# Kernel optimization log

Measured on AMD Instinct MI355X. Metric: run time of the kernel, lower is better.

Reference implementation:

```python
import jax, jax.numpy as jnp
import numpy as np

T, B, E, H, R = 1024, 8, 1024, 16, 16
HD = E // H


def setup_inputs() -> dict:
    key = jax.random.key(0)
    ks = jax.random.split(key, 10)
    w = lambda k, shape: (jax.random.normal(k, shape, jnp.float32) * 0.02)
    return {
        "query": jax.random.normal(ks[0], (T, B, E), jnp.float32),
        "in_proj_weight": w(ks[1], (3 * E, E)),
        "in_proj_bias": jnp.zeros((3 * E,), jnp.float32),
        "in_left": w(ks[2], (3 * E, R)),   # LrkLinear(rank -> 3E) weight
        "in_right": w(ks[3], (R, E)),      # LrkLinear(E -> rank) weight
        "out_proj_weight": w(ks[4], (E, E)),
        "out_proj_bias": jnp.zeros((E,), jnp.float32),
        "out_left": w(ks[5], (E, R)),
        "out_right": w(ks[6], (R, E)),
        "rel_pos_bias": w(ks[7], (H, T, T)),
    }


def reference(query, in_proj_weight, in_proj_bias, in_left, in_right,
              out_proj_weight, out_proj_bias, out_left, out_right, rel_pos_bias):
    t, b, e = query.shape
    hd = e // H
    scaling = float(hd) ** -0.5
    # fused in-projection: residual full-rank + low-rank branch
    acti = (jnp.einsum('tbe,fe->tbf', query, in_proj_weight) + in_proj_bias
            + jnp.einsum('tbr,fr->tbf', jnp.einsum('tbe,re->tbr', query, in_right), in_left))
    q, k, v = jnp.split(acti, 3, axis=-1)
    q = q * scaling
    # (T,B,E) -> (B,H,T,hd); matches torch view(T, B*H, hd).transpose(0,1)
    to_heads = lambda x: x.reshape(t, b, H, hd).transpose(1, 2, 0, 3)
    qh, kh, vh = to_heads(q), to_heads(k), to_heads(v)
    scores = jnp.einsum('bhtd,bhsd->bhts', qh, kh) + rel_pos_bias  # bias broadcasts over batch
    attn = jax.nn.softmax(scores, axis=-1)  # dropout_p = 0
    out = jnp.einsum('bhts,bhsd->bhtd', attn, vh)
    out = out.transpose(2, 0, 1, 3).reshape(t, b, e)
    # out-projection: residual full-rank + low-rank branch
    out = (jnp.einsum('tbe,fe->tbf', out, out_proj_weight) + out_proj_bias
           + jnp.einsum('tbr,fr->tbf', jnp.einsum('tbe,re->tbr', out, out_right), out_left))
    return out
```

## Files before the change

kernel.cpp:

```cpp
#include <hip/hip_runtime.h>
#include <hip/hip_bf16.h>


typedef __attribute__((ext_vector_type(8))) __bf16 bf16x8;
typedef __attribute__((ext_vector_type(4))) float f32x4;

__device__ __forceinline__ float bf2f(unsigned short u) {
  union { unsigned int i; float f; } v; v.i = ((unsigned int)u) << 16; return v.f;
}
__device__ __forceinline__ unsigned short f2bf(float f) {
  union { float f; unsigned int i; } v; v.f = f;
  unsigned int x = v.i;
  unsigned int r = x + 0x7FFFu + ((x >> 16) & 1u);
  return (unsigned short)(r >> 16);
}
__device__ __forceinline__ unsigned int pack2(float a, float b) {
  return (unsigned int)f2bf(a) | ((unsigned int)f2bf(b) << 16);
}
__device__ __forceinline__ float ld_in(const void* p, long idx, int isf32) {
  if (isf32) return ((const float*)p)[idx];
  return bf2f(((const unsigned short*)p)[idx]);
}
__device__ __forceinline__ void gl_lds16(const unsigned short* g, unsigned short* l) {
  __builtin_amdgcn_global_load_lds(
      (const __attribute__((address_space(1))) unsigned int*)g,
      (__attribute__((address_space(3))) unsigned int*)l, 16, 0, 0);
}

__global__ void detect_kernel(const unsigned int* __restrict__ q, int* __restrict__ flag) {
  __shared__ int cnt;
  if (threadIdx.x == 0) cnt = 0;
  __syncthreads();
  unsigned int w = q[threadIdx.x];
  int c = 0;
  if (((w >> 7) & 0xFFu) >= 0xC0u) c++;
  if (((w >> 23) & 0xFFu) >= 0xC0u) c++;
  atomicAdd(&cnt, c);
  __syncthreads();
  if (threadIdx.x == 0) flag[0] = (cnt >= 2) ? 1 : 0;
}

__global__ __launch_bounds__(256) void convert_bf16(
    const void* __restrict__ in, unsigned short* __restrict__ out,
    const int* __restrict__ flag) {
  long idx = ((long)blockIdx.x * 256 + threadIdx.x) * 8;
  if (flag[0]) {
    const float* p = (const float*)in + idx;
    float4 a = ((const float4*)p)[0], b = ((const float4*)p)[1];
    uint4 v;
    v.x = pack2(a.x, a.y); v.y = pack2(a.z, a.w);
    v.z = pack2(b.x, b.y); v.w = pack2(b.z, b.w);
    *(uint4*)(out + idx) = v;
  } else {
    *(uint4*)(out + idx) = *(const uint4*)((const unsigned short*)in + idx);
  }
}

__global__ __launch_bounds__(256) void eff_weights(
    const void* __restrict__ w, const void* __restrict__ left,
    const void* __restrict__ right, unsigned short* __restrict__ outw,
    const int* __restrict__ flag) {
  const int isf32 = flag[0];
  long idx = (long)blockIdx.x * 256 + threadIdx.x;
  long f = idx >> 10, e = idx & 1023;
  float acc = ld_in(w, idx, isf32);
#pragma unroll
  for (int r = 0; r < 16; ++r)
    acc += ld_in(left, (f << 4) + r, isf32) * ld_in(right, (r << 10) + e, isf32);
  outw[idx] = f2bf(acc);
}

__global__ __launch_bounds__(256) void inproj_kernel(
    const unsigned short* __restrict__ qbf,
    const unsigned short* __restrict__ weff,
    const void* __restrict__ bias,
    unsigned short* __restrict__ qh, unsigned short* __restrict__ kh,
    unsigned short* __restrict__ vt, const int* __restrict__ flag) {
  __shared__ __align__(16) unsigned short As[128 * 32];
  __shared__ __align__(16) unsigned short Bs[128 * 32];
  const int isf32 = flag[0];
  const int tid = threadIdx.x;
  const int wave = tid >> 6, lane = tid & 63, quad = lane >> 4, lrow = lane & 15;
  const int wr0 = (wave >> 1) * 64, wc0 = (wave & 1) * 64;
  const int fbase = blockIdx.x * 128, mbase = blockIdx.y * 128;
  const int srow = lane >> 2, scol = (lane & 3) * 8;
  const unsigned short* ag  = qbf  + (long)(mbase + 32 * wave + srow) * 1024 + scol;
  const unsigned short* ag2 = ag + 16 * 1024;
  const unsigned short* bg  = weff + (long)(fbase + 32 * wave + srow) * 1024 + scol;
  const unsigned short* bg2 = bg + 16 * 1024;
  unsigned short* la  = &As[(32 * wave) * 32];
  unsigned short* la2 = &As[(32 * wave + 16) * 32];
  unsigned short* lb  = &Bs[(32 * wave) * 32];
  unsigned short* lb2 = &Bs[(32 * wave + 16) * 32];

  f32x4 acc[4][4] = {};
  for (int k0 = 0; k0 < 1024; k0 += 32) {
    gl_lds16(ag + k0, la);
    gl_lds16(ag2 + k0, la2);
    gl_lds16(bg + k0, lb);
    gl_lds16(bg2 + k0, lb2);
    __syncthreads();
    bf16x8 af[4], bfv[4];
#pragma unroll
    for (int mi = 0; mi < 4; ++mi)
      af[mi] = *(const bf16x8*)&As[(wr0 + mi * 16 + lrow) * 32 + quad * 8];
#pragma unroll
    for (int ni = 0; ni < 4; ++ni)
      bfv[ni] = *(const bf16x8*)&Bs[(wc0 + ni * 16 + lrow) * 32 + quad * 8];
#pragma unroll
    for (int mi = 0; mi < 4; ++mi)
#pragma unroll
      for (int ni = 0; ni < 4; ++ni)
        acc[mi][ni] = __builtin_amdgcn_mfma_f32_16x16x32_bf16(af[mi], bfv[ni], acc[mi][ni], 0, 0, 0);
    __syncthreads();
  }
  const int which = fbase >> 10;
  const int h = ((fbase + wc0) >> 6) & 15;
#pragma unroll
  for (int ni = 0; ni < 4; ++ni) {
    const int d = ni * 16 + lrow;
    const float bv = ld_in(bias, fbase + wc0 + d, isf32);
#pragma unroll
    for (int mi = 0; mi < 4; ++mi)
#pragma unroll
      for (int r = 0; r < 4; ++r) {
        const int m = mbase + wr0 + mi * 16 + quad * 4 + r;
        const int t = m >> 3, b = m & 7;
        const float val = acc[mi][ni][r] + bv;
        if (which == 0)
          qh[((long)(b * 16 + h) * 1024 + t) * 64 + d] = f2bf(val * 0.125f);
        else if (which == 1)
          kh[((long)(b * 16 + h) * 1024 + t) * 64 + d] = f2bf(val);
        else
          vt[((long)(b * 16 + h) * 64 + d) * 1024 + t] = f2bf(val);
      }
  }
}

__global__ __launch_bounds__(256) void attn_kernel(
    const unsigned short* __restrict__ qh, const unsigned short* __restrict__ kh,
    const unsigned short* __restrict__ vt, const void* __restrict__ rpb,
    const unsigned short* __restrict__ pre,
    unsigned short* __restrict__ ctx, const int* __restrict__ flag) {
  __shared__ __align__(16) unsigned short Ks[2 * 64 * 32];
  __shared__ __align__(16) unsigned short Ps[4][16][72];
  const int isf32 = flag[0];
  const int tid = threadIdx.x;
  const int wave = tid >> 6, lane = tid & 63, quad = lane >> 4, lrow = lane & 15;
  const int bh = blockIdx.y, b = bh >> 4, h = bh & 15;
  const int t0 = blockIdx.x * 64;

  const unsigned short* qbase = qh + ((long)(bh * 1024) + t0 + wave * 16 + lrow) * 64;
  bf16x8 qf0 = *(const bf16x8*)(qbase + quad * 8);
  bf16x8 qf1 = *(const bf16x8*)(qbase + 32 + quad * 8);

  const unsigned short* kbase = kh + (long)bh * 65536;
  const unsigned short* vbase = vt + (long)bh * 65536;

  const long bidx0 = ((long)h * 1024 + t0 + wave * 16 + quad * 4) * 1024 + lrow;
  const unsigned short* bs16 = pre ? pre : (const unsigned short*)rpb;
  const bool bf32 = (isf32 && pre == nullptr);
  const float* bsf = (const float*)rpb;

  const int j0 = 2 * wave, j1 = 2 * wave + 1;
  const int kk0 = j0 >> 2, ii0 = j0 & 3, kk1 = j1 >> 2, ii1 = j1 & 3;
  const unsigned short* kg0 = kbase + (long)(16 * ii0 + (lane >> 2)) * 64 + kk0 * 32 + (lane & 3) * 8;
  const unsigned short* kg1 = kbase + (long)(16 * ii1 + (lane >> 2)) * 64 + kk1 * 32 + (lane & 3) * 8;
  unsigned short* lk0 = &Ks[kk0 * 2048 + ii0 * 512];
  unsigned short* lk1 = &Ks[kk1 * 2048 + ii1 * 512];

  f32x4 oacc[4] = {};
  float rsum[4] = {0.f, 0.f, 0.f, 0.f};

  for (int s0 = 0; s0 < 1024; s0 += 64) {
    gl_lds16(kg0 + (long)s0 * 64, lk0);
    gl_lds16(kg1 + (long)s0 * 64, lk1);
    __syncthreads();

    float bia[4][4];
    if (bf32) {
#pragma unroll
      for (int r = 0; r < 4; ++r)
#pragma unroll
        for (int n = 0; n < 4; ++n)
          bia[r][n] = bsf[bidx0 + r * 1024 + s0 + n * 16];
    } else {
#pragma unroll
      for (int r = 0; r < 4; ++r)
#pragma unroll
        for (int n = 0; n < 4; ++n)
          bia[r][n] = bf2f(bs16[bidx0 + r * 1024 + s0 + n * 16]);
    }

    f32x4 sacc[4] = {};
#pragma unroll
    for (int n = 0; n < 4; ++n) {
      bf16x8 kf0 = *(const bf16x8*)&Ks[(n * 16 + lrow) * 32 + quad * 8];
      bf16x8 kf1 = *(const bf16x8*)&Ks[2048 + (n * 16 + lrow) * 32 + quad * 8];
      sacc[n] = __builtin_amdgcn_mfma_f32_16x16x32_bf16(qf0, kf0, sacc[n], 0, 0, 0);
      sacc[n] = __builtin_amdgcn_mfma_f32_16x16x32_bf16(qf1, kf1, sacc[n], 0, 0, 0);
    }

#pragma unroll
    for (int n = 0; n < 4; ++n)
#pragma unroll
      for (int r = 0; r < 4; ++r) {
        float p = __expf(sacc[n][r] + bia[r][n]);
        rsum[r] += p;
        Ps[wave][quad * 4 + r][n * 16 + lrow] = f2bf(p);
      }

    asm volatile("s_waitcnt lgkmcnt(0)" ::: "memory");

#pragma unroll
    for (int kk = 0; kk < 2; ++kk) {
      bf16x8 pf = *(const bf16x8*)&Ps[wave][lrow][kk * 32 + quad * 8];
#pragma unroll
      for (int n = 0; n < 4; ++n) {
        bf16x8 vf = *(const bf16x8*)(vbase + (long)(n * 16 + lrow) * 1024 + s0 + kk * 32 + quad * 8);
        oacc[n] = __builtin_amdgcn_mfma_f32_16x16x32_bf16(pf, vf, oacc[n], 0, 0, 0);
      }
    }
    __syncthreads();
  }

#pragma unroll
  for (int msk = 1; msk <= 8; msk <<= 1)
#pragma unroll
    for (int r = 0; r < 4; ++r)
      rsum[r] += __shfl_xor(rsum[r], msk, 64);

  float linv[4];
#pragma unroll
  for (int r = 0; r < 4; ++r) linv[r] = 1.0f / rsum[r];
#pragma unroll
  for (int n = 0; n < 4; ++n)
#pragma unroll
    for (int r = 0; r < 4; ++r) {
      const int t = t0 + wave * 16 + quad * 4 + r;
      ctx[((long)t * 8 + b) * 1024 + h * 64 + n * 16 + lrow] = f2bf(oacc[n][r] * linv[r]);
    }
}

__global__ __launch_bounds__(256) void outproj_kernel(
    const unsigned short* __restrict__ ctx, const unsigned short* __restrict__ weff,
    const void* __restrict__ bias, void* __restrict__ out,
    const int* __restrict__ flag) {
  __shared__ __align__(16) unsigned short As[128 * 32];
  __shared__ __align__(16) unsigned short Bs[128 * 32];
  const int isf32 = flag[0];
  const int tid = threadIdx.x;
  const int wave = tid >> 6, lane = tid & 63, quad = lane >> 4, lrow = lane & 15;
  const int wr0 = (wave >> 1) * 64, wc0 = (wave & 1) * 64;
  const int fbase = blockIdx.x * 128, mbase = blockIdx.y * 128;
  const int srow = lane >> 2, scol = (lane & 3) * 8;
  const unsigned short* ag  = ctx  + (long)(mbase + 32 * wave + srow) * 1024 + scol;
  const unsigned short* ag2 = ag + 16 * 1024;
  const unsigned short* bg  = weff + (long)(fbase + 32 * wave + srow) * 1024 + scol;
  const unsigned short* bg2 = bg + 16 * 1024;
  unsigned short* la  = &As[(32 * wave) * 32];
  unsigned short* la2 = &As[(32 * wave + 16) * 32];
  unsigned short* lb  = &Bs[(32 * wave) * 32];
  unsigned short* lb2 = &Bs[(32 * wave + 16) * 32];

  f32x4 acc[4][4] = {};
  for (int k0 = 0; k0 < 1024; k0 += 32) {
    gl_lds16(ag + k0, la);
    gl_lds16(ag2 + k0, la2);
    gl_lds16(bg + k0, lb);
    gl_lds16(bg2 + k0, lb2);
    __syncthreads();
    bf16x8 af[4], bfv[4];
#pragma unroll
    for (int mi = 0; mi < 4; ++mi)
      af[mi] = *(const bf16x8*)&As[(wr0 + mi * 16 + lrow) * 32 + quad * 8];
#pragma unroll
    for (int ni = 0; ni < 4; ++ni)
      bfv[ni] = *(const bf16x8*)&Bs[(wc0 + ni * 16 + lrow) * 32 + quad * 8];
#pragma unroll
    for (int mi = 0; mi < 4; ++mi)
#pragma unroll
      for (int ni = 0; ni < 4; ++ni)
        acc[mi][ni] = __builtin_amdgcn_mfma_f32_16x16x32_bf16(af[mi], bfv[ni], acc[mi][ni], 0, 0, 0);
    __syncthreads();
  }
#pragma unroll
  for (int ni = 0; ni < 4; ++ni) {
    const int f = fbase + wc0 + ni * 16 + lrow;
    const float bv = ld_in(bias, f, isf32);
#pragma unroll
    for (int mi = 0; mi < 4; ++mi)
#pragma unroll
      for (int r = 0; r < 4; ++r) {
        const int m = mbase + wr0 + mi * 16 + quad * 4 + r;
        const float val = acc[mi][ni][r] + bv;
        if (isf32) ((float*)out)[(long)m * 1024 + f] = val;
        else       ((unsigned short*)out)[(long)m * 1024 + f] = f2bf(val);
      }
  }
}

extern "C" void kernel_launch(void* const* d_in, const int* in_sizes, int n_in,
                              void* d_out, int out_size, void* d_ws, size_t ws_size,
                              hipStream_t stream) {
  (void)out_size;
  static const int EXP[10] = {8388608, 3145728, 3072, 49152, 16384,
                              1048576, 1024, 16384, 16384, 16777216};
  if (n_in != 10) return;
  for (int i = 0; i < 10; ++i) if (in_sizes[i] != EXP[i]) return;

  const void* query = d_in[0];
  const void* ipw = d_in[1];  const void* ipb = d_in[2];
  const void* il  = d_in[3];  const void* ir  = d_in[4];
  const void* opw = d_in[5];  const void* opb = d_in[6];
  const void* ol  = d_in[7];  const void* orr = d_in[8];
  const void* rpb = d_in[9];

  int* flag = (int*)d_ws;
  unsigned short* base = (unsigned short*)d_ws + 16;
  unsigned short* w_in_eff  = base;
  unsigned short* w_out_eff = w_in_eff + (long)3072 * 1024;
  unsigned short* qh  = w_out_eff + (long)1024 * 1024;
  unsigned short* kh  = qh + 8388608L;
  unsigned short* vt  = kh + 8388608L;
  unsigned short* ctx = vt + 8388608L;
  unsigned short* rpbbf = ctx + 8388608L;
  unsigned short* qbf = ctx;
  const size_t NEED_FULL = 32 + (3145728L + 1048576L + 4L * 8388608L + 16777216L) * 2;
  const bool big = ws_size >= NEED_FULL;

  detect_kernel<<<dim3(1), dim3(64), 0, stream>>>((const unsigned int*)query, flag);
  if (big)
    convert_bf16<<<dim3(8192), dim3(256), 0, stream>>>(rpb, rpbbf, flag);
  convert_bf16<<<dim3(4096), dim3(256), 0, stream>>>(query, qbf, flag);
  eff_weights<<<dim3(12288), dim3(256), 0, stream>>>(ipw, il, ir, w_in_eff, flag);
  eff_weights<<<dim3(4096), dim3(256), 0, stream>>>(opw, ol, orr, w_out_eff, flag);
  inproj_kernel<<<dim3(24, 64), dim3(256), 0, stream>>>(qbf, w_in_eff, ipb, qh, kh, vt, flag);
  attn_kernel<<<dim3(16, 128), dim3(256), 0, stream>>>(qh, kh, vt, rpb,
                                                       big ? rpbbf : nullptr, ctx, flag);
  outproj_kernel<<<dim3(8, 64), dim3(256), 0, stream>>>(ctx, w_out_eff, opb, d_out, flag);
}
```

Measured before the change: 495.0 us.

## Double-buffer K/V tiles in LDS and prefetch bias in attention loop

Moves V loads from direct global reads into LDS via async global_load_lds, double-buffers both K and V tiles so the next tile loads while the current one computes, and prefetches the relative-position bias one iteration ahead in registers. It also XOR-swizzles the P scratch layout to cut LDS bank conflicts and reorders blockIdx.y so that blocks sharing a head, and hence the same bias rows, run close together for better cache reuse. This doubles LDS use and raises register pressure, which may lower occupancy.

```diff
diff --git a/kernel.cpp b/kernel.cpp
--- a/kernel.cpp
+++ b/kernel.cpp
@@ -142,12 +142,13 @@
     const unsigned short* __restrict__ vt, const void* __restrict__ rpb,
     const unsigned short* __restrict__ pre,
     unsigned short* __restrict__ ctx, const int* __restrict__ flag) {
-  __shared__ __align__(16) unsigned short Ks[2 * 64 * 32];
-  __shared__ __align__(16) unsigned short Ps[4][16][72];
+  __shared__ __align__(16) unsigned short Ks[2][4096];
+  __shared__ __align__(16) unsigned short Vs[2][4096];
+  __shared__ __align__(16) unsigned short Ps[4][1024];
   const int isf32 = flag[0];
   const int tid = threadIdx.x;
   const int wave = tid >> 6, lane = tid & 63, quad = lane >> 4, lrow = lane & 15;
-  const int bh = blockIdx.y, b = bh >> 4, h = bh & 15;
+  const int b = blockIdx.y & 7, h = blockIdx.y >> 3, bh = b * 16 + h;
   const int t0 = blockIdx.x * 64;
 
   const unsigned short* qbase = qh + ((long)(bh * 1024) + t0 + wave * 16 + lrow) * 64;
@@ -162,41 +163,67 @@
   const bool bf32 = (isf32 && pre == nullptr);
   const float* bsf = (const float*)rpb;
 
-  const int j0 = 2 * wave, j1 = 2 * wave + 1;
+  const int j0 = 2 * wave, j1 = j0 + 1;
   const int kk0 = j0 >> 2, ii0 = j0 & 3, kk1 = j1 >> 2, ii1 = j1 & 3;
-  const unsigned short* kg0 = kbase + (long)(16 * ii0 + (lane >> 2)) * 64 + kk0 * 32 + (lane & 3) * 8;
-  const unsigned short* kg1 = kbase + (long)(16 * ii1 + (lane >> 2)) * 64 + kk1 * 32 + (lane & 3) * 8;
-  unsigned short* lk0 = &Ks[kk0 * 2048 + ii0 * 512];
-  unsigned short* lk1 = &Ks[kk1 * 2048 + ii1 * 512];
+  const int sr = lane >> 2, sc = (lane & 3) * 8;
+  const unsigned short* kg0 = kbase + (long)(16 * ii0 + sr) * 64 + kk0 * 32 + sc;
+  const unsigned short* kg1 = kbase + (long)(16 * ii1 + sr) * 64 + kk1 * 32 + sc;
+  const unsigned short* vg0 = vbase + (long)(16 * ii0 + sr) * 1024 + kk0 * 32 + sc;
+  const unsigned short* vg1 = vbase + (long)(16 * ii1 + sr) * 1024 + kk1 * 32 + sc;
+  const int lo0 = kk0 * 2048 + ii0 * 512, lo1 = kk1 * 2048 + ii1 * 512;
 
   f32x4 oacc[4] = {};
   float rsum[4] = {0.f, 0.f, 0.f, 0.f};
-
-  for (int s0 = 0; s0 < 1024; s0 += 64) {
-    gl_lds16(kg0 + (long)s0 * 64, lk0);
-    gl_lds16(kg1 + (long)s0 * 64, lk1);
-    __syncthreads();
-
-    float bia[4][4];
-    if (bf32) {
-#pragma unroll
-      for (int r = 0; r < 4; ++r)
-#pragma unroll
-        for (int n = 0; n < 4; ++n)
-          bia[r][n] = bsf[bidx0 + r * 1024 + s0 + n * 16];
-    } else {
-#pragma unroll
-      for (int r = 0; r < 4; ++r)
-#pragma unroll
-        for (int n = 0; n < 4; ++n)
-          bia[r][n] = bf2f(bs16[bidx0 + r * 1024 + s0 + n * 16]);
+  unsigned int bcur[4][4], bnxt[4][4];
+
+  gl_lds16(kg0, &Ks[0][lo0]);
+  gl_lds16(kg1, &Ks[0][lo1]);
+  gl_lds16(vg0, &Vs[0][lo0]);
+  gl_lds16(vg1, &Vs[0][lo1]);
+  if (bf32) {
+#pragma unroll
+    for (int r = 0; r < 4; ++r)
+#pragma unroll
+      for (int n = 0; n < 4; ++n)
+        bcur[r][n] = __float_as_uint(bsf[bidx0 + r * 1024 + n * 16]);
+  } else {
+#pragma unroll
+    for (int r = 0; r < 4; ++r)
+#pragma unroll
+      for (int n = 0; n < 4; ++n)
+        bcur[r][n] = (unsigned int)bs16[bidx0 + r * 1024 + n * 16];
+  }
+  __syncthreads();
+
+  for (int t = 0; t < 16; ++t) {
+    const int cur = t & 1;
+    const int s0 = t << 6;
+    if (t < 15) {
+      const int sn = s0 + 64;
+      gl_lds16(kg0 + (long)sn * 64, &Ks[cur ^ 1][lo0]);
+      gl_lds16(kg1 + (long)sn * 64, &Ks[cur ^ 1][lo1]);
+      gl_lds16(vg0 + sn, &Vs[cur ^ 1][lo0]);
+      gl_lds16(vg1 + sn, &Vs[cur ^ 1][lo1]);
+      if (bf32) {
+#pragma unroll
+        for (int r = 0; r < 4; ++r)
+#pragma unroll
+          for (int n = 0; n < 4; ++n)
+            bnxt[r][n] = __float_as_uint(bsf[bidx0 + r * 1024 + sn + n * 16]);
+      } else {
+#pragma unroll
+        for (int r = 0; r < 4; ++r)
+#pragma unroll
+          for (int n = 0; n < 4; ++n)
+            bnxt[r][n] = (unsigned int)bs16[bidx0 + r * 1024 + sn + n * 16];
+      }
     }
 
     f32x4 sacc[4] = {};
 #pragma unroll
     for (int n = 0; n < 4; ++n) {
-      bf16x8 kf0 = *(const bf16x8*)&Ks[(n * 16 + lrow) * 32 + quad * 8];
-      bf16x8 kf1 = *(const bf16x8*)&Ks[2048 + (n * 16 + lrow) * 32 + quad * 8];
+      bf16x8 kf0 = *(const bf16x8*)&Ks[cur][(n * 16 + lrow) * 32 + quad * 8];
+      bf16x8 kf1 = *(const bf16x8*)&Ks[cur][2048 + (n * 16 + lrow) * 32 + quad * 8];
       sacc[n] = __builtin_amdgcn_mfma_f32_16x16x32_bf16(qf0, kf0, sacc[n], 0, 0, 0);
       sacc[n] = __builtin_amdgcn_mfma_f32_16x16x32_bf16(qf1, kf1, sacc[n], 0, 0, 0);
     }
@@ -205,23 +232,32 @@
     for (int n = 0; n < 4; ++n)
 #pragma unroll
       for (int r = 0; r < 4; ++r) {
-        float p = __expf(sacc[n][r] + bia[r][n]);
+        const int row = quad * 4 + r;
+        const float bv = bf32 ? __uint_as_float(bcur[r][n])
+                              : bf2f((unsigned short)bcur[r][n]);
+        const float p = __expf(sacc[n][r] + bv);
         rsum[r] += p;
-        Ps[wave][quad * 4 + r][n * 16 + lrow] = f2bf(p);
+        Ps[wave][(row * 64 + n * 16 + lrow) ^ ((row & 7) << 3)] = f2bf(p);
       }
 
     asm volatile("s_waitcnt lgkmcnt(0)" ::: "memory");
 
 #pragma unroll
     for (int kk = 0; kk < 2; ++kk) {
-      bf16x8 pf = *(const bf16x8*)&Ps[wave][lrow][kk * 32 + quad * 8];
+      bf16x8 pf = *(const bf16x8*)&Ps[wave][(lrow * 64 + kk * 32 + quad * 8) ^ ((lrow & 7) << 3)];
 #pragma unroll
       for (int n = 0; n < 4; ++n) {
-        bf16x8 vf = *(const bf16x8*)(vbase + (long)(n * 16 + lrow) * 1024 + s0 + kk * 32 + quad * 8);
+        bf16x8 vf = *(const bf16x8*)&Vs[cur][kk * 2048 + (n * 16 + lrow) * 32 + quad * 8];
         oacc[n] = __builtin_amdgcn_mfma_f32_16x16x32_bf16(pf, vf, oacc[n], 0, 0, 0);
       }
     }
     __syncthreads();
+    if (t < 15) {
+#pragma unroll
+      for (int r = 0; r < 4; ++r)
+#pragma unroll
+        for (int n = 0; n < 4; ++n) bcur[r][n] = bnxt[r][n];
+    }
   }
 
 #pragma unroll
```

New measurement: 432.4 us. 1.14x faster.
